# Performance work log

Hardware: AMD Instinct MI355X
Metric: run time of the kernel (lower is better)

Reference implementation:

```python
import jax, jax.numpy as jnp
import numpy as np

B, N, D, H = 4, 4096, 512, 512
EDGE_P = 0.01  # adjacency density


def _glorot(key, shape):
    fan_in, fan_out = shape
    limit = np.sqrt(6.0 / (fan_in + fan_out)).astype(np.float32)
    return jax.random.uniform(key, shape, jnp.float32, -limit, limit)


def setup_inputs() -> dict:
    key = jax.random.key(0)
    ks = jax.random.split(key, 9)
    batch_graph = jax.random.normal(ks[0], (B, N, D), jnp.float32)
    adj = (jax.random.uniform(ks[1], (B, N, N)) < EDGE_P).astype(jnp.float32)
    adj = jnp.minimum(adj + jnp.eye(N, dtype=jnp.float32)[None], 1.0)  # self loops, 0/1
    return {
        "batch_graph": batch_graph,
        "adj": adj,
        "W1": _glorot(ks[2], (D, H)), "b1": jnp.zeros((H,), jnp.float32),
        "W2": _glorot(ks[3], (H, H)), "b2": jnp.zeros((H,), jnp.float32),
        "W3": _glorot(ks[4], (H, D)), "b3": jnp.zeros((D,), jnp.float32),
    }


def _normalize_adj(adj):
    # Faithful to GCN.normalize_sparse_adj: D^{-1/2} A^T D^{-1/2}
    rowsum = adj.sum(axis=1)                       # [B, N] (sum over dim 1, as in torch)
    d_inv_sqrt = jnp.where(rowsum > 0, jax.lax.rsqrt(jnp.maximum(rowsum, 1e-30)), 0.0)
    # (A @ diag(d))^T @ diag(d)  ->  d_i * A[j,i] * d_j
    return d_inv_sqrt[:, :, None] * jnp.swapaxes(adj, 1, 2) * d_inv_sqrt[:, None, :]


def reference(batch_graph, adj, W1, b1, W2, b2, W3, b3):
    # Block-diagonal big_adj @ big_graph == independent per-batch matmuls;
    # we exploit that instead of materializing the [B*N, B*N] dense matrix.
    a = _normalize_adj(adj)                                   # [B, N, N]
    # GraphConvolution (pygcn-style): out = adj @ (x @ W) + b; dropout = identity (eval)
    h = jax.nn.relu(jnp.einsum('bij,bjd->bid', a, batch_graph @ W1) + b1)
    h = jax.nn.relu(jnp.einsum('bij,bjd->bid', a, h @ W2) + b2)
    out = jnp.einsum('bij,bjd->bid', a, h @ W3) + b3          # [B, N, D]
    return out
```

## Files before the change

### kernel.cpp

```cpp
#include <hip/hip_runtime.h>
#include <stdint.h>

#define PCAP 64
#define RPB 4

typedef __attribute__((ext_vector_type(8))) short bf16x8;
typedef __attribute__((ext_vector_type(4))) float f32x4;

typedef __attribute__((address_space(3))) uint32_t lds_u32;
typedef __attribute__((address_space(1))) const uint32_t glb_u32;

__device__ __forceinline__ unsigned short f2bf(float f) {
  union { float f; uint32_t u; } c; c.f = f;
  return (unsigned short)((c.u + 0x7fffu + ((c.u >> 16) & 1u)) >> 16);
}
__device__ __forceinline__ float bf2f(uint32_t b) {
  union { uint32_t u; float f; } c; c.u = b << 16; return c.f;
}
__device__ __forceinline__ float as_f32(uint32_t u) {
  union { uint32_t u; float f; } c; c.u = u; return c.f;
}

__global__ __launch_bounds__(256) void k_detect(const uint32_t* __restrict__ a,
                                                int* __restrict__ flag) {
  int i = blockIdx.x * 256 + threadIdx.x;
  bool found = false;
  for (int k = 0; k < 64; k++) {
    uint32_t x = a[(size_t)k * 65536 + i];
    if (x == 0x00003F80u || x == 0x3F803F80u) found = true;
  }
  if (found) flag[0] = 1;
}

__global__ __launch_bounds__(256) void k_build(const void* __restrict__ adjp,
                                               int* __restrict__ cnt4,
                                               int* __restrict__ cols4,
                                               const int* __restrict__ flag) {
  int gid = blockIdx.x * 256 + threadIdx.x;
  if (flag[0]) {
    const uint4* a = (const uint4*)adjp;
    uint4 v = a[gid];
    int i0 = (gid & 511) * 8;
    int j  = (gid >> 9) & 4095;
    int b  = gid >> 21;
    int base = b << 12;
    int panel = j >> 10;
    uint32_t w[4] = {v.x, v.y, v.z, v.w};
#pragma unroll
    for (int q = 0; q < 4; q++) {
      if (w[q] & 0xffffu) {
        int c = base + i0 + q * 2;
        int p = atomicAdd(&cnt4[c * 4 + panel], 1);
        if (p < PCAP) cols4[((size_t)(c * 4 + panel) << 6) + p] = j;
      }
      if (w[q] >> 16) {
        int c = base + i0 + q * 2 + 1;
        int p = atomicAdd(&cnt4[c * 4 + panel], 1);
        if (p < PCAP) cols4[((size_t)(c * 4 + panel) << 6) + p] = j;
      }
    }
  } else {
    const float4* a = (const float4*)adjp;
#pragma unroll
    for (int it = 0; it < 2; it++) {
      int v4 = gid + it * 8388608;
      float4 v = a[v4];
      int i0 = (v4 & 1023) * 4;
      int j  = (v4 >> 10) & 4095;
      int b  = v4 >> 22;
      int base = b << 12;
      int panel = j >> 10;
      float e[4] = {v.x, v.y, v.z, v.w};
#pragma unroll
      for (int q = 0; q < 4; q++) {
        if (e[q] != 0.0f) {
          int c = base + i0 + q;
          int p = atomicAdd(&cnt4[c * 4 + panel], 1);
          if (p < PCAP) cols4[((size_t)(c * 4 + panel) << 6) + p] = j;
        }
      }
    }
  }
}

__global__ __launch_bounds__(256) void k_post(const void* __restrict__ xp,
                                              ushort* __restrict__ xb,
                                              const void* w1, const void* w2,
                                              const void* w3,
                                              ushort* __restrict__ wt1,
                                              ushort* __restrict__ wt2,
                                              ushort* __restrict__ wt3,
                                              const int* __restrict__ cnt4,
                                              float* __restrict__ dinv,
                                              const void* b1, const void* b2,
                                              const void* b3,
                                              float* __restrict__ b1f,
                                              float* __restrict__ b2f,
                                              float* __restrict__ b3f,
                                              const int* __restrict__ flag) {
  int B = blockIdx.x;
  int t = threadIdx.x;
  if (B < 4096) {
    int gid = B * 256 + t;
    if (flag[0]) {
      ((uint4*)xb)[gid] = ((const uint4*)xp)[gid];
    } else {
      const float4* in = (const float4*)xp;
#pragma unroll
      for (int it = 0; it < 2; it++) {
        int i = gid + it * 1048576;
        float4 v = in[i];
        uint32_t lo = (uint32_t)f2bf(v.x) | ((uint32_t)f2bf(v.y) << 16);
        uint32_t hi = (uint32_t)f2bf(v.z) | ((uint32_t)f2bf(v.w) << 16);
        ((uint2*)xb)[i] = make_uint2(lo, hi);
      }
    }
  } else if (B < 7168) {
    int id = (B - 4096) * 256 + t;
    int w = id >> 18;
    int o = id & 262143;
    const void* wp = (w == 0) ? w1 : (w == 1) ? w2 : w3;
    ushort* wt = (w == 0) ? wt1 : (w == 1) ? wt2 : wt3;
    int n = o >> 9, k = o & 511;
    if (flag[0]) wt[o] = ((const ushort*)wp)[k * 512 + n];
    else         wt[o] = f2bf(((const float*)wp)[k * 512 + n]);
  } else {
    int id = (B - 7168) * 256 + t;
    if (id < 16384) {
      int4 cc = ((const int4*)cnt4)[id];
      int s = cc.x + cc.y + cc.z + cc.w;
      dinv[id] = (s > 0) ? 1.0f / sqrtf((float)s) : 0.0f;
    } else {
      int o = id - 16384;
      if (o < 1536) {
        const void* src = (o < 512) ? b1 : (o < 1024) ? b2 : b3;
        float* dst = (o < 512) ? b1f : (o < 1024) ? b2f : b3f;
        int i = o & 511;
        dst[i] = flag[0] ? bf2f(((const ushort*)src)[i]) : ((const float*)src)[i];
      }
    }
  }
}

__device__ __forceinline__ void gl_lds16(const ushort* g, ushort* l) {
  __builtin_amdgcn_global_load_lds((glb_u32*)g, (lds_u32*)l, 16, 0, 0);
}

__global__ __launch_bounds__(256) void k_gemm(const ushort* __restrict__ X,
                                              const ushort* __restrict__ WT,
                                              ushort* __restrict__ Z) {
  __shared__ ushort As[128 * 32];
  __shared__ ushort Bs[128 * 32];
  const int K = 512, NO = 512;
  int tid = threadIdx.x;
  int m0 = blockIdx.y * 128, n0 = blockIdx.x * 128;
  int lane = tid & 63;
  int wv = tid >> 6;
  int wm = (wv >> 1) << 6;
  int wn = (wv & 1) << 6;
  int lr = lane & 15;
  int lq = lane >> 4;

  f32x4 zero = {0.f, 0.f, 0.f, 0.f};
  f32x4 acc[4][4];
#pragma unroll
  for (int im = 0; im < 4; im++)
#pragma unroll
    for (int in_ = 0; in_ < 4; in_++) acc[im][in_] = zero;

  const ushort* Xg = X  + (size_t)(m0 + (tid >> 2)) * K + ((tid & 3) << 3);
  const ushort* Wg = WT + (size_t)(n0 + (tid >> 2)) * K + ((tid & 3) << 3);

  for (int kt = 0; kt < K; kt += 32) {
    __syncthreads();
    gl_lds16(Xg + kt,                    &As[tid * 8]);
    gl_lds16(Xg + kt + (size_t)64 * K,   &As[2048 + tid * 8]);
    gl_lds16(Wg + kt,                    &Bs[tid * 8]);
    gl_lds16(Wg + kt + (size_t)64 * K,   &Bs[2048 + tid * 8]);
    __syncthreads();
    bf16x8 af[4], bfr[4];
#pragma unroll
    for (int im = 0; im < 4; im++)
      af[im] = *(const bf16x8*)&As[(wm + im * 16 + lr) * 32 + lq * 8];
#pragma unroll
    for (int in_ = 0; in_ < 4; in_++)
      bfr[in_] = *(const bf16x8*)&Bs[(wn + in_ * 16 + lr) * 32 + lq * 8];
#pragma unroll
    for (int im = 0; im < 4; im++)
#pragma unroll
      for (int in_ = 0; in_ < 4; in_++)
        acc[im][in_] = __builtin_amdgcn_mfma_f32_16x16x32_bf16(
            af[im], bfr[in_], acc[im][in_], 0, 0, 0);
  }

#pragma unroll
  for (int im = 0; im < 4; im++) {
    int row0 = m0 + wm + im * 16 + lq * 4;
#pragma unroll
    for (int in_ = 0; in_ < 4; in_++) {
      int col = n0 + wn + in_ * 16 + lr;
#pragma unroll
      for (int r = 0; r < 4; r++)
        Z[(size_t)(row0 + r) * NO + col] = f2bf(acc[im][in_][r]);
    }
  }
}

__global__ __launch_bounds__(256) void k_spmm(const ushort* __restrict__ Z,
                                              const int* __restrict__ cnt4,
                                              const int* __restrict__ cols4,
                                              const float* __restrict__ dinv,
                                              const float* __restrict__ bias,
                                              void* __restrict__ outp,
                                              int do_relu, int is_final,
                                              const int* __restrict__ flag) {
  int B = blockIdx.x;
  int wv = threadIdx.x >> 6;
  int lane = threadIdx.x & 63;
  int batch = (B & 7) >> 1;
  int lb = ((B >> 3) << 1) | (B & 1);
  int r = (batch << 12) + lb * RPB + wv;
  int base = batch << 12;

  float dr = dinv[r];
  const ushort* Zb = Z + (size_t)base * 512 + lane * 8;
  const float4* bp = (const float4*)bias + lane * 2;
  float4 bb0 = bp[0], bb1 = bp[1];
  float a[8] = {bb0.x, bb0.y, bb0.z, bb0.w, bb1.x, bb1.y, bb1.z, bb1.w};

#pragma unroll
  for (int p = 0; p < 4; p++) {
    int nz = cnt4[r * 4 + p];
    if (nz > PCAP) nz = PCAP;
    int jl = 0; float vl = 0.f;
    if (lane < nz) {
      jl = cols4[((size_t)(r * 4 + p) << 6) + lane];
      vl = dr * dinv[base + jl];
    }
    int k = 0;
    for (; k + 2 <= nz; k += 2) {
      int   j0 = __shfl(jl, k),     j1 = __shfl(jl, k + 1);
      float v0 = __shfl(vl, k),     v1 = __shfl(vl, k + 1);
      uint4 z0 = *(const uint4*)(Zb + (size_t)j0 * 512);
      uint4 z1 = *(const uint4*)(Zb + (size_t)j1 * 512);
      uint32_t w0[4] = {z0.x, z0.y, z0.z, z0.w};
      uint32_t w1[4] = {z1.x, z1.y, z1.z, z1.w};
#pragma unroll
      for (int q = 0; q < 4; q++) {
        a[q * 2]     += v0 * as_f32(w0[q] << 16);
        a[q * 2 + 1] += v0 * as_f32(w0[q] & 0xffff0000u);
        a[q * 2]     += v1 * as_f32(w1[q] << 16);
        a[q * 2 + 1] += v1 * as_f32(w1[q] & 0xffff0000u);
      }
    }
    if (k < nz) {
      int   j0 = __shfl(jl, k);
      float v0 = __shfl(vl, k);
      uint4 z0 = *(const uint4*)(Zb + (size_t)j0 * 512);
      uint32_t w0[4] = {z0.x, z0.y, z0.z, z0.w};
#pragma unroll
      for (int q = 0; q < 4; q++) {
        a[q * 2]     += v0 * as_f32(w0[q] << 16);
        a[q * 2 + 1] += v0 * as_f32(w0[q] & 0xffff0000u);
      }
    }
  }

  if (do_relu) {
#pragma unroll
    for (int q = 0; q < 8; q++) a[q] = fmaxf(a[q], 0.f);
  }

  if (!is_final || flag[0]) {
    uint4 o;
    o.x = (uint32_t)f2bf(a[0]) | ((uint32_t)f2bf(a[1]) << 16);
    o.y = (uint32_t)f2bf(a[2]) | ((uint32_t)f2bf(a[3]) << 16);
    o.z = (uint32_t)f2bf(a[4]) | ((uint32_t)f2bf(a[5]) << 16);
    o.w = (uint32_t)f2bf(a[6]) | ((uint32_t)f2bf(a[7]) << 16);
    *(uint4*)((ushort*)outp + (size_t)r * 512 + lane * 8) = o;
  } else {
    float4* op = (float4*)((float*)outp + (size_t)r * 512 + lane * 8);
    op[0] = make_float4(a[0], a[1], a[2], a[3]);
    op[1] = make_float4(a[4], a[5], a[6], a[7]);
  }
}

extern "C" void kernel_launch(void* const* d_in, const int* in_sizes, int n_in,
                              void* d_out, int out_size, void* d_ws, size_t ws_size,
                              hipStream_t stream) {
  const void* X  = d_in[0];
  const void* A  = d_in[1];
  const void* W1 = d_in[2]; const void* b1 = d_in[3];
  const void* W2 = d_in[4]; const void* b2 = d_in[5];
  const void* W3 = d_in[6]; const void* b3 = d_in[7];

  char* ws = (char*)d_ws;
  size_t off = 0;
  auto alloc = [&](size_t bytes) -> void* {
    void* p = ws + off;
    off += (bytes + 255) & ~(size_t)255;
    return p;
  };
  int*    cnt4 = (int*)alloc((size_t)16384 * 4 * 4);
  int*    flag = (int*)alloc(4);
  float*  dinv = (float*)alloc(16384 * 4);
  int*    cols4= (int*)alloc((size_t)16384 * 4 * PCAP * 4);
  ushort* W1T  = (ushort*)alloc(512 * 512 * 2);
  ushort* W2T  = (ushort*)alloc(512 * 512 * 2);
  ushort* W3T  = (ushort*)alloc(512 * 512 * 2);
  float*  b1f  = (float*)alloc(512 * 4);
  float*  b2f  = (float*)alloc(512 * 4);
  float*  b3f  = (float*)alloc(512 * 4);
  ushort* Xb   = (ushort*)alloc((size_t)16384 * 512 * 2);
  ushort* Zb   = (ushort*)alloc((size_t)16384 * 512 * 2);
  ushort* Hb   = (ushort*)alloc((size_t)16384 * 512 * 2);

  hipMemsetAsync(cnt4, 0, 262144 + 256, stream);

  k_detect<<<256, 256, 0, stream>>>((const uint32_t*)A, flag);
  k_build<<<32768, 256, 0, stream>>>(A, cnt4, cols4, flag);
  k_post<<<7238, 256, 0, stream>>>(X, Xb, W1, W2, W3, W1T, W2T, W3T,
                                   cnt4, dinv, b1, b2, b3, b1f, b2f, b3f, flag);

  dim3 gg(4, 128);
  k_gemm<<<gg, 256, 0, stream>>>(Xb, W1T, Zb);
  k_spmm<<<4096, 256, 0, stream>>>(Zb, cnt4, cols4, dinv, b1f, Hb, 1, 0, flag);
  k_gemm<<<gg, 256, 0, stream>>>(Hb, W2T, Zb);
  k_spmm<<<4096, 256, 0, stream>>>(Zb, cnt4, cols4, dinv, b2f, Xb, 1, 0, flag);
  k_gemm<<<gg, 256, 0, stream>>>(Xb, W3T, Zb);
  k_spmm<<<4096, 256, 0, stream>>>(Zb, cnt4, cols4, dinv, b3f, d_out, 0, 1, flag);
}
```

Measured before the change: 612.4 us.

## Restructure SpMM to stage column slices of Z in LDS per block

The SpMM kernel is rewritten. Each block now owns 512 rows and a 32-column slice of one batch. It stages 1024-row tiles of Z into LDS with global_load_lds, then each thread accumulates 16 rows by walking their column lists against the LDS tile. The aim is to replace the scattered 1 KB row gathers from global memory with reads from on-chip storage. In exchange the column lists are reread once per column slice, threads in a wave diverge because their nonzero counts differ, and only 512 blocks with a large per-thread accumulator array are launched. Two smaller changes ride along: adjacency reads in the build kernel become nontemporal loads, and the redundant bf16 copy of the input is skipped by letting the first GEMM read the raw input when it is already bf16.

After: 1.144 ms. +86.8%, slower.

```diff
diff --git a/kernel.cpp b/kernel.cpp
--- a/kernel.cpp
+++ b/kernel.cpp
@@ -2,10 +2,10 @@
 #include <stdint.h>
 
 #define PCAP 64
-#define RPB 4
 
 typedef __attribute__((ext_vector_type(8))) short bf16x8;
 typedef __attribute__((ext_vector_type(4))) float f32x4;
+typedef __attribute__((ext_vector_type(4))) uint32_t u32x4;
 
 typedef __attribute__((address_space(3))) uint32_t lds_u32;
 typedef __attribute__((address_space(1))) const uint32_t glb_u32;
@@ -38,8 +38,8 @@
                                                const int* __restrict__ flag) {
   int gid = blockIdx.x * 256 + threadIdx.x;
   if (flag[0]) {
-    const uint4* a = (const uint4*)adjp;
-    uint4 v = a[gid];
+    const u32x4* a = (const u32x4*)adjp;
+    u32x4 v = __builtin_nontemporal_load(&a[gid]);
     int i0 = (gid & 511) * 8;
     int j  = (gid >> 9) & 4095;
     int b  = gid >> 21;
@@ -60,11 +60,11 @@
       }
     }
   } else {
-    const float4* a = (const float4*)adjp;
+    const f32x4* a = (const f32x4*)adjp;
 #pragma unroll
     for (int it = 0; it < 2; it++) {
       int v4 = gid + it * 8388608;
-      float4 v = a[v4];
+      f32x4 v = __builtin_nontemporal_load(&a[v4]);
       int i0 = (v4 & 1023) * 4;
       int j  = (v4 >> 10) & 4095;
       int b  = v4 >> 22;
@@ -101,19 +101,16 @@
   int B = blockIdx.x;
   int t = threadIdx.x;
   if (B < 4096) {
+    if (flag[0]) return;
     int gid = B * 256 + t;
-    if (flag[0]) {
-      ((uint4*)xb)[gid] = ((const uint4*)xp)[gid];
-    } else {
-      const float4* in = (const float4*)xp;
-#pragma unroll
-      for (int it = 0; it < 2; it++) {
-        int i = gid + it * 1048576;
-        float4 v = in[i];
-        uint32_t lo = (uint32_t)f2bf(v.x) | ((uint32_t)f2bf(v.y) << 16);
-        uint32_t hi = (uint32_t)f2bf(v.z) | ((uint32_t)f2bf(v.w) << 16);
-        ((uint2*)xb)[i] = make_uint2(lo, hi);
-      }
+    const float4* in = (const float4*)xp;
+#pragma unroll
+    for (int it = 0; it < 2; it++) {
+      int i = gid + it * 1048576;
+      float4 v = in[i];
+      uint32_t lo = (uint32_t)f2bf(v.x) | ((uint32_t)f2bf(v.y) << 16);
+      uint32_t hi = (uint32_t)f2bf(v.z) | ((uint32_t)f2bf(v.w) << 16);
+      ((uint2*)xb)[i] = make_uint2(lo, hi);
     }
   } else if (B < 7168) {
     int id = (B - 4096) * 256 + t;
@@ -146,12 +143,15 @@
   __builtin_amdgcn_global_load_lds((glb_u32*)g, (lds_u32*)l, 16, 0, 0);
 }
 
-__global__ __launch_bounds__(256) void k_gemm(const ushort* __restrict__ X,
+__global__ __launch_bounds__(256) void k_gemm(const void* __restrict__ Xraw,
+                                              const ushort* __restrict__ Xconv,
                                               const ushort* __restrict__ WT,
-                                              ushort* __restrict__ Z) {
+                                              ushort* __restrict__ Z,
+                                              const int* __restrict__ flag) {
   __shared__ ushort As[128 * 32];
   __shared__ ushort Bs[128 * 32];
   const int K = 512, NO = 512;
+  const ushort* X = flag[0] ? (const ushort*)Xraw : Xconv;
   int tid = threadIdx.x;
   int m0 = blockIdx.y * 128, n0 = blockIdx.x * 128;
   int lane = tid & 63;
@@ -206,82 +206,90 @@
   }
 }
 
-__global__ __launch_bounds__(256) void k_spmm(const ushort* __restrict__ Z,
-                                              const int* __restrict__ cnt4,
-                                              const int* __restrict__ cols4,
-                                              const float* __restrict__ dinv,
-                                              const float* __restrict__ bias,
-                                              void* __restrict__ outp,
-                                              int do_relu, int is_final,
-                                              const int* __restrict__ flag) {
-  int B = blockIdx.x;
-  int wv = threadIdx.x >> 6;
-  int lane = threadIdx.x & 63;
-  int batch = (B & 7) >> 1;
-  int lb = ((B >> 3) << 1) | (B & 1);
-  int r = (batch << 12) + lb * RPB + wv;
-  int base = batch << 12;
-
-  float dr = dinv[r];
-  const ushort* Zb = Z + (size_t)base * 512 + lane * 8;
-  const float4* bp = (const float4*)bias + lane * 2;
-  float4 bb0 = bp[0], bb1 = bp[1];
-  float a[8] = {bb0.x, bb0.y, bb0.z, bb0.w, bb1.x, bb1.y, bb1.z, bb1.w};
-
-#pragma unroll
-  for (int p = 0; p < 4; p++) {
-    int nz = cnt4[r * 4 + p];
-    if (nz > PCAP) nz = PCAP;
-    int jl = 0; float vl = 0.f;
-    if (lane < nz) {
-      jl = cols4[((size_t)(r * 4 + p) << 6) + lane];
-      vl = dr * dinv[base + jl];
-    }
-    int k = 0;
-    for (; k + 2 <= nz; k += 2) {
-      int   j0 = __shfl(jl, k),     j1 = __shfl(jl, k + 1);
-      float v0 = __shfl(vl, k),     v1 = __shfl(vl, k + 1);
-      uint4 z0 = *(const uint4*)(Zb + (size_t)j0 * 512);
-      uint4 z1 = *(const uint4*)(Zb + (size_t)j1 * 512);
-      uint32_t w0[4] = {z0.x, z0.y, z0.z, z0.w};
-      uint32_t w1[4] = {z1.x, z1.y, z1.z, z1.w};
-#pragma unroll
-      for (int q = 0; q < 4; q++) {
-        a[q * 2]     += v0 * as_f32(w0[q] << 16);
-        a[q * 2 + 1] += v0 * as_f32(w0[q] & 0xffff0000u);
-        a[q * 2]     += v1 * as_f32(w1[q] << 16);
-        a[q * 2 + 1] += v1 * as_f32(w1[q] & 0xffff0000u);
-      }
-    }
-    if (k < nz) {
-      int   j0 = __shfl(jl, k);
-      float v0 = __shfl(vl, k);
-      uint4 z0 = *(const uint4*)(Zb + (size_t)j0 * 512);
-      uint32_t w0[4] = {z0.x, z0.y, z0.z, z0.w};
-#pragma unroll
-      for (int q = 0; q < 4; q++) {
-        a[q * 2]     += v0 * as_f32(w0[q] << 16);
-        a[q * 2 + 1] += v0 * as_f32(w0[q] & 0xffff0000u);
-      }
-    }
-  }
-
-  if (do_relu) {
-#pragma unroll
-    for (int q = 0; q < 8; q++) a[q] = fmaxf(a[q], 0.f);
-  }
-
-  if (!is_final || flag[0]) {
-    uint4 o;
-    o.x = (uint32_t)f2bf(a[0]) | ((uint32_t)f2bf(a[1]) << 16);
-    o.y = (uint32_t)f2bf(a[2]) | ((uint32_t)f2bf(a[3]) << 16);
-    o.z = (uint32_t)f2bf(a[4]) | ((uint32_t)f2bf(a[5]) << 16);
-    o.w = (uint32_t)f2bf(a[6]) | ((uint32_t)f2bf(a[7]) << 16);
-    *(uint4*)((ushort*)outp + (size_t)r * 512 + lane * 8) = o;
-  } else {
-    float4* op = (float4*)((float*)outp + (size_t)r * 512 + lane * 8);
-    op[0] = make_float4(a[0], a[1], a[2], a[3]);
-    op[1] = make_float4(a[4], a[5], a[6], a[7]);
+__global__ __launch_bounds__(256, 2) void k_spmm(const ushort* __restrict__ Z,
+                                                 const int* __restrict__ cnt4,
+                                                 const int* __restrict__ cols4,
+                                                 const float* __restrict__ dinv,
+                                                 const float* __restrict__ bias,
+                                                 void* __restrict__ outp,
+                                                 int do_relu, int is_final,
+                                                 const int* __restrict__ flag) {
+  __shared__ ushort Zt[1024 * 32];
+  int Bk = blockIdx.x;
+  int b  = Bk >> 7;
+  int rb = (Bk >> 4) & 7;
+  int cs = Bk & 15;
+  int t = threadIdx.x;
+  int lane = t & 63, w = t >> 6;
+  int base = b << 12;
+  int c0 = cs << 5;
+  int tr = t >> 3;
+  int tc = (t & 7) << 2;
+
+  float acc[16][4];
+#pragma unroll
+  for (int rc = 0; rc < 16; rc++)
+#pragma unroll
+    for (int q = 0; q < 4; q++) acc[rc][q] = 0.f;
+
+  const ushort* Zg = Z + (size_t)base * 512;
+
+  for (int tile = 0; tile < 4; tile++) {
+    int jbase = tile << 10;
+#pragma unroll
+    for (int it = 0; it < 16; it++) {
+      int jj0 = (w << 8) + (it << 4);
+      int jj = jj0 + (lane >> 2);
+      gl_lds16(Zg + (size_t)(jbase + jj) * 512 + c0 + ((lane & 3) << 3),
+               &Zt[(size_t)jj * 32 + ((lane & 3) << 3)]);
+    }
+    __syncthreads();
+#pragma unroll 1
+    for (int rc = 0; rc < 16; rc++) {
+      int row = (rb << 9) + (rc << 5) + tr;
+      int r = base + row;
+      int slot = (r << 2) + tile;
+      int nnz = cnt4[slot];
+      if (nnz > PCAP) nnz = PCAP;
+      const int* cl = &cols4[(size_t)slot << 6];
+      for (int e = 0; e < nnz; e++) {
+        int j = cl[e];
+        float v = dinv[base + j];
+        int jj = j & 1023;
+        uint2 zz = *(const uint2*)&Zt[jj * 32 + tc];
+        acc[rc][0] += v * as_f32(zz.x << 16);
+        acc[rc][1] += v * as_f32(zz.x & 0xffff0000u);
+        acc[rc][2] += v * as_f32(zz.y << 16);
+        acc[rc][3] += v * as_f32(zz.y & 0xffff0000u);
+      }
+    }
+    __syncthreads();
+  }
+
+  float bb[4];
+#pragma unroll
+  for (int q = 0; q < 4; q++) bb[q] = bias[c0 + tc + q];
+
+#pragma unroll 1
+  for (int rc = 0; rc < 16; rc++) {
+    int row = (rb << 9) + (rc << 5) + tr;
+    int r = base + row;
+    float dr = dinv[r];
+    float o[4];
+#pragma unroll
+    for (int q = 0; q < 4; q++) {
+      o[q] = acc[rc][q] * dr + bb[q];
+      if (do_relu) o[q] = fmaxf(o[q], 0.f);
+    }
+    if (!is_final || flag[0]) {
+      uint2 pk;
+      pk.x = (uint32_t)f2bf(o[0]) | ((uint32_t)f2bf(o[1]) << 16);
+      pk.y = (uint32_t)f2bf(o[2]) | ((uint32_t)f2bf(o[3]) << 16);
+      *(uint2*)((ushort*)outp + (size_t)r * 512 + c0 + tc) = pk;
+    } else {
+      *(float4*)((float*)outp + (size_t)r * 512 + c0 + tc) =
+          make_float4(o[0], o[1], o[2], o[3]);
+    }
   }
 }
 
@@ -315,7 +323,7 @@
   ushort* Zb   = (ushort*)alloc((size_t)16384 * 512 * 2);
   ushort* Hb   = (ushort*)alloc((size_t)16384 * 512 * 2);
 
-  hipMemsetAsync(cnt4, 0, 262144 + 256, stream);
+  (void)hipMemsetAsync(cnt4, 0, 262144 + 256, stream);
 
   k_detect<<<256, 256, 0, stream>>>((const uint32_t*)A, flag);
   k_build<<<32768, 256, 0, stream>>>(A, cnt4, cols4, flag);
@@ -323,10 +331,10 @@
                                    cnt4, dinv, b1, b2, b3, b1f, b2f, b3f, flag);
 
   dim3 gg(4, 128);
-  k_gemm<<<gg, 256, 0, stream>>>(Xb, W1T, Zb);
-  k_spmm<<<4096, 256, 0, stream>>>(Zb, cnt4, cols4, dinv, b1f, Hb, 1, 0, flag);
-  k_gemm<<<gg, 256, 0, stream>>>(Hb, W2T, Zb);
-  k_spmm<<<4096, 256, 0, stream>>>(Zb, cnt4, cols4, dinv, b2f, Xb, 1, 0, flag);
-  k_gemm<<<gg, 256, 0, stream>>>(Xb, W3T, Zb);
-  k_spmm<<<4096, 256, 0, stream>>>(Zb, cnt4, cols4, dinv, b3f, d_out, 0, 1, flag);
-}
+  k_gemm<<<gg, 256, 0, stream>>>(X, Xb, W1T, Zb, flag);
+  k_spmm<<<512, 256, 0, stream>>>(Zb, cnt4, cols4, dinv, b1f, Hb, 1, 0, flag);
+  k_gemm<<<gg, 256, 0, stream>>>(Hb, Hb, W2T, Zb, flag);
+  k_spmm<<<512, 256, 0, stream>>>(Zb, cnt4, cols4, dinv, b2f, Xb, 1, 0, flag);
+  k_gemm<<<gg, 256, 0, stream>>>(Xb, Xb, W3T, Zb, flag);
+  k_spmm<<<512, 256, 0, stream>>>(Zb, cnt4, cols4, dinv, b3f, d_out, 0, 1, flag);
+}
```
